# Kernel tuning notes

Measured on AMD Instinct MI355X. Metric: run time of the kernel, lower is better.

## Reference

```python
import jax, jax.numpy as jnp
import numpy as np

HALF_WIN = 6  # window_size // 2 on each side (window_size=13)


def setup_inputs() -> dict:
    key = jax.random.key(0)
    k1, k2, k3 = jax.random.split(key, 3)
    B, N, C = 2, 4096, 768
    x = jax.random.normal(k1, (B, N, C), dtype=jnp.float32)
    # torch Linear init ~ U(-1/sqrt(in), 1/sqrt(in)); stored here as [in, out]
    s = 1.0 / np.sqrt(C)
    w_qkv = jax.random.uniform(k2, (C, 3 * C), jnp.float32, -s, s)
    w_proj = jax.random.uniform(k3, (C, C), jnp.float32, -s, s)
    b_proj = jnp.zeros((C,), jnp.float32)
    return {"x": x, "w_qkv": w_qkv, "w_proj": w_proj, "b_proj": b_proj}


def _local_attn(x, w_qkv, w_proj, b_proj, num_heads=12):
    B, N, C = x.shape
    H = num_heads
    D = C // H
    W = 2 * HALF_WIN + 1  # 13

    qkv = (x @ w_qkv).reshape(B, N, 3, H, D)
    q, k, v = qkv[:, :, 0], qkv[:, :, 1], qkv[:, :, 2]  # each [B,N,H,D]

    # sliding-window gather: for each query i, keys at i-6..i+6
    offs = jnp.arange(-HALF_WIN, HALF_WIN + 1)            # [W]
    idx = jnp.arange(N)[:, None] + offs[None, :]          # [N,W]
    valid = (idx >= 0) & (idx < N)                        # [N,W]
    idxc = jnp.clip(idx, 0, N - 1)

    k_win = k[:, idxc]  # [B,N,W,H,D]
    v_win = v[:, idxc]  # [B,N,W,H,D]

    scale = D ** (-0.5)  # xformers default softmax scale
    scores = jnp.einsum('bnhd,bnwhd->bnhw', q, k_win) * scale  # [B,N,H,W]
    neg = jnp.asarray(jnp.finfo(scores.dtype).min, scores.dtype)
    scores = jnp.where(valid[None, :, None, :], scores, neg)
    p = jax.nn.softmax(scores, axis=-1)

    out = jnp.einsum('bnhw,bnwhd->bnhd', p, v_win)  # [B,N,H,D]
    out = out.reshape(B, N, C)
    return out @ w_proj + b_proj


def reference(x, w_qkv, w_proj, b_proj):
    return _local_attn(x, w_qkv, w_proj, b_proj)
```

## Files before the change

kernel.cpp:

```cpp
#include <hip/hip_runtime.h>

typedef unsigned short u16;
typedef unsigned int u32;
typedef __attribute__((ext_vector_type(8))) short short8;
typedef __attribute__((ext_vector_type(4))) float f32x4;

#define GLOBAL_AS(p) (const __attribute__((address_space(1))) void*)(p)
#define LDS_AS(p) (__attribute__((address_space(3))) void*)(p)

__device__ __forceinline__ u16 f2b(float f) {
  u32 u = __float_as_uint(f);
  u32 r = (u + 0x7fffu + ((u >> 16) & 1u)) >> 16;
  return (u16)r;
}
__device__ __forceinline__ float blo(u32 u) { return __uint_as_float(u << 16); }
__device__ __forceinline__ float bhi(u32 u) { return __uint_as_float(u & 0xffff0000u); }

__global__ void conv_bf16(const float* __restrict__ in, u16* __restrict__ out, int n4) {
  int i = blockIdx.x * blockDim.x + threadIdx.x;
  int stride = gridDim.x * blockDim.x;
  for (; i < n4; i += stride) {
    float4 f = ((const float4*)in)[i];
    ushort4 u;
    u.x = f2b(f.x); u.y = f2b(f.y); u.z = f2b(f.z); u.w = f2b(f.w);
    ((ushort4*)out)[i] = u;
  }
}

__global__ void transpose_conv2(const float* __restrict__ w_qkv, u16* __restrict__ wqT,
                                const float* __restrict__ w_proj, u16* __restrict__ wpT) {
  __shared__ float tile[32][33];
  const int z = blockIdx.z;
  if (z && blockIdx.x >= 24) return;
  const float* in = z ? w_proj : w_qkv;
  u16* out = z ? wpT : wqT;
  const int Cc = z ? 768 : 2304;
  int c0 = blockIdx.x * 32, r0 = blockIdx.y * 32;
  int tx = threadIdx.x, ty = threadIdx.y;
#pragma unroll
  for (int i = 0; i < 32; i += 8)
    tile[ty + i][tx] = in[(size_t)(r0 + ty + i) * Cc + c0 + tx];
  __syncthreads();
#pragma unroll
  for (int i = 0; i < 32; i += 8)
    out[(size_t)(c0 + ty + i) * 768 + r0 + tx] = f2b(tile[tx][ty + i]);
}


#define GLD(SRC, DST) __builtin_amdgcn_global_load_lds(GLOBAL_AS(SRC), LDS_AS(DST), 16, 0, 0)
#define WAITN(n) asm volatile("s_waitcnt vmcnt(" #n ")" ::: "memory")

#define WAITSEL                                                                          \
  do {                                                                                   \
    if (NBCH >= 1024) { if (wex) WAITN(7); else WAITN(6); }                              \
    else              { if (wex) WAITN(6); else WAITN(5); }                              \
  } while (0)

#define STAGEW(KT, SB)                                                                   \
  do {                                                                                   \
    const u16* a_ = gA0 + (KT) * 64;                                                     \
    GLD(a_,            lA + (SB) * 16384 + t * 8);                                       \
    GLD(a_ + 64 * kk,  lA + (SB) * 16384 + (t + 512) * 8);                               \
    GLD(a_ + 128 * kk, lA + (SB) * 16384 + (t + 1024) * 8);                              \
    GLD(a_ + 192 * kk, lA + (SB) * 16384 + (t + 1536) * 8);                              \
    const u16* b_ = gB0 + (KT) * 64;                                                     \
    GLD(b_, lB + (SB) * TBSZ + t * 8);                                                   \
    if (NBCH >= 1024) {                                                                  \
      GLD(b_ + 64 * kk, lB + (SB) * TBSZ + (t + 512) * 8);                               \
      if (t < NBCH - 1024) GLD(b_ + 128 * kk, lB + (SB) * TBSZ + (t + 1024) * 8);        \
    } else {                                                                             \
      if (t < NBCH - 512) GLD(b_ + 64 * kk, lB + (SB) * TBSZ + (t + 512) * 8);           \
    }                                                                                    \
  } while (0)

#define ITERW(KT, CB, SB, DOSTAGE, FINAL)                                                \
  do {                                                                                   \
    if (FINAL) WAITN(0); else WAITSEL;                                                   \
    __builtin_amdgcn_s_barrier();                                                        \
    asm volatile("" ::: "memory");                                                       \
    if (DOSTAGE) STAGEW((KT) + 2, SB);                                                   \
    const u16* pa_ = lA + (CB) * 16384;                                                  \
    const u16* pb_ = lB + (CB) * TBSZ;                                                   \
    {                                                                                    \
      short8 a0 = *(const short8*)(pa_ + arow0 + cs0);                                   \
      short8 a1 = *(const short8*)(pa_ + arow1 + cs0);                                   \
      short8 bf[NFRAG];                                                                  \
      _Pragma("unroll")                                                                  \
      for (int ni = 0; ni < NFRAG; ++ni)                                                 \
        bf[ni] = *(const short8*)(pb_ + ni * 1024 + browb + cs0);                        \
      __builtin_amdgcn_s_setprio(1);                                                     \
      _Pragma("unroll")                                                                  \
      for (int ni = 0; ni < NFRAG; ++ni) {                                               \
        acc[0][ni] = __builtin_amdgcn_mfma_f32_16x16x32_bf16(a0, bf[ni], acc[0][ni], 0, 0, 0); \
        acc[1][ni] = __builtin_amdgcn_mfma_f32_16x16x32_bf16(a1, bf[ni], acc[1][ni], 0, 0, 0); \
      }                                                                                  \
      __builtin_amdgcn_s_setprio(0);                                                     \
    }                                                                                    \
    {                                                                                    \
      short8 a0 = *(const short8*)(pa_ + arow0 + cs1);                                   \
      short8 a1 = *(const short8*)(pa_ + arow1 + cs1);                                   \
      short8 bf[NFRAG];                                                                  \
      _Pragma("unroll")                                                                  \
      for (int ni = 0; ni < NFRAG; ++ni)                                                 \
        bf[ni] = *(const short8*)(pb_ + ni * 1024 + browb + cs1);                        \
      __builtin_amdgcn_s_setprio(1);                                                     \
      _Pragma("unroll")                                                                  \
      for (int ni = 0; ni < NFRAG; ++ni) {                                               \
        acc[0][ni] = __builtin_amdgcn_mfma_f32_16x16x32_bf16(a0, bf[ni], acc[0][ni], 0, 0, 0); \
        acc[1][ni] = __builtin_amdgcn_mfma_f32_16x16x32_bf16(a1, bf[ni], acc[1][ni], 0, 0, 0); \
      }                                                                                  \
      __builtin_amdgcn_s_setprio(0);                                                     \
    }                                                                                    \
  } while (0)

template <int EPI, int NFRAG>
__global__ __launch_bounds__(512, 2) void gemmW(
    const u16* __restrict__ A, const u16* __restrict__ Bt, void* __restrict__ Cout,
    const float* __restrict__ bias, int M, int N, int K, int NXP) {
  constexpr int NBCH = NFRAG * 128;
  constexpr int TBSZ = NFRAG * 1024;
  constexpr int EXW = (NBCH >= 1024 ? NBCH - 1024 : NBCH - 512) / 64;
  extern __shared__ u16 sm[];
  u16* lA = sm;
  u16* lB = sm + 3 * 16384;
  const int t = threadIdx.x;
  const size_t kk = (size_t)K;
  const int nwg = gridDim.x;
  const int logical = (blockIdx.x & 7) * (nwg >> 3) + (blockIdx.x >> 3);
  const int m0 = (logical / NXP) * 256;
  const int n0 = (logical % NXP) * (NFRAG * 16);
  const int wv = t >> 6, l = t & 63;
  const int lr = l & 15, g = l >> 4;
  const bool wex = wv < EXW;

  const int ra = t >> 3;
  const int ca = (t & 7) ^ (ra & 7);
  const u16* gA0 = A + (size_t)(m0 + ra) * kk + ca * 8;
  const u16* gB0 = Bt + (size_t)(n0 + ra) * kk + ca * 8;

  const int cs0 = ((g + 0) ^ (lr & 7)) * 8;
  const int cs1 = ((g + 4) ^ (lr & 7)) * 8;
  const int arow0 = (wv * 32 + lr) * 64, arow1 = (wv * 32 + 16 + lr) * 64;
  const int browb = lr * 64;

  f32x4 acc[2][NFRAG] = {};

  STAGEW(0, 0);
  STAGEW(1, 1);
  for (int j = 0; j < 3; ++j) {
    const int kt = j * 3;
    ITERW(kt + 0, 0, 2, 1, 0);
    ITERW(kt + 1, 1, 0, 1, 0);
    ITERW(kt + 2, 2, 1, 1, 0);
  }
  ITERW(9, 0, 2, 1, 0);
  ITERW(10, 1, 2, 0, 0);
  ITERW(11, 2, 2, 0, 1);

#pragma unroll
  for (int mi = 0; mi < 2; ++mi) {
    int row = m0 + wv * 32 + mi * 16 + g * 4;
#pragma unroll
    for (int ni = 0; ni < NFRAG; ++ni) {
      int col = n0 + ni * 16 + lr;
#pragma unroll
      for (int r = 0; r < 4; ++r) {
        float v = acc[mi][ni][r];
        if (EPI == 0) {
          ((u16*)Cout)[(size_t)(row + r) * N + col] = f2b(v);
        } else {
          ((float*)Cout)[(size_t)(row + r) * N + col] = v + bias[col];
        }
      }
    }
  }
}

#define NTILE 128
#define ROWS 140
#define LPAD 66

__global__ __launch_bounds__(512, 6) void attn_kernel(const u16* __restrict__ qkv,
                                                      u16* __restrict__ attn) {
  const int nt = blockIdx.x, h = blockIdx.y, b = blockIdx.z;
  const int n0 = nt * NTILE;
  const int t = threadIdx.x;
  __shared__ u16 kl[ROWS * LPAD];
  __shared__ u16 vl[ROWS * LPAD];

  for (int i = t; i < 2 * ROWS * 8; i += 512) {
    int mat = i >= ROWS * 8;
    int j = mat ? i - ROWS * 8 : i;
    int r = j >> 3, c = j & 7;
    int grow = n0 - 6 + r;
    grow = grow < 0 ? 0 : (grow > 4095 ? 4095 : grow);
    const uint4 u =
        *(const uint4*)(qkv + (size_t)(b * 4096 + grow) * 2304 + (mat ? 1536 : 768) + h * 64 + c * 8);
    u16* dst = (mat ? vl : kl) + r * LPAD + c * 8;
    ((u32*)dst)[0] = u.x;
    ((u32*)dst)[1] = u.y;
    ((u32*)dst)[2] = u.z;
    ((u32*)dst)[3] = u.w;
  }
  __syncthreads();

  const int r = t >> 2;
  const int p = t & 3;
  const int n = n0 + r;
  const int dbase = p * 16;

  float qf[16];
  const u16* qp = qkv + (size_t)(b * 4096 + n) * 2304 + h * 64 + dbase;
#pragma unroll
  for (int c = 0; c < 2; ++c) {
    uint4 u = *(const uint4*)(qp + c * 8);
    qf[c * 8 + 0] = blo(u.x); qf[c * 8 + 1] = bhi(u.x);
    qf[c * 8 + 2] = blo(u.y); qf[c * 8 + 3] = bhi(u.y);
    qf[c * 8 + 4] = blo(u.z); qf[c * 8 + 5] = bhi(u.z);
    qf[c * 8 + 6] = blo(u.w); qf[c * 8 + 7] = bhi(u.w);
  }

  float s[13];
#pragma unroll
  for (int w = 0; w < 13; ++w) s[w] = 0.f;
#pragma unroll
  for (int d2 = 0; d2 < 8; ++d2) {
    float q0 = qf[2 * d2], q1 = qf[2 * d2 + 1];
#pragma unroll
    for (int w = 0; w < 13; ++w) {
      u32 u = *(const u32*)(kl + (r + w) * LPAD + dbase + 2 * d2);
      s[w] += q0 * blo(u) + q1 * bhi(u);
    }
  }
#pragma unroll
  for (int w = 0; w < 13; ++w) {
    s[w] += __shfl_xor(s[w], 1);
    s[w] += __shfl_xor(s[w], 2);
  }

#pragma unroll
  for (int w = 0; w < 13; ++w) {
    int nn = n - 6 + w;
    s[w] = (nn >= 0 && nn < 4096) ? s[w] * 0.125f : -1e30f;
  }
  float m = s[0];
#pragma unroll
  for (int w = 1; w < 13; ++w) m = fmaxf(m, s[w]);
  float sum = 0.f;
#pragma unroll
  for (int w = 0; w < 13; ++w) {
    float pr = __expf(s[w] - m);
    s[w] = pr;
    sum += pr;
  }
  float inv = 1.0f / sum;

  float o[16];
#pragma unroll
  for (int d = 0; d < 16; ++d) o[d] = 0.f;
#pragma unroll
  for (int w = 0; w < 13; ++w) {
    float pw = s[w] * inv;
#pragma unroll
    for (int d2 = 0; d2 < 8; ++d2) {
      u32 u = *(const u32*)(vl + (r + w) * LPAD + dbase + 2 * d2);
      o[2 * d2] += pw * blo(u);
      o[2 * d2 + 1] += pw * bhi(u);
    }
  }

  u16* op = attn + (size_t)(b * 4096 + n) * 768 + h * 64 + dbase;
#pragma unroll
  for (int c = 0; c < 2; ++c) {
    uint4 u;
    u.x = (u32)f2b(o[c * 8 + 0]) | ((u32)f2b(o[c * 8 + 1]) << 16);
    u.y = (u32)f2b(o[c * 8 + 2]) | ((u32)f2b(o[c * 8 + 3]) << 16);
    u.z = (u32)f2b(o[c * 8 + 4]) | ((u32)f2b(o[c * 8 + 5]) << 16);
    u.w = (u32)f2b(o[c * 8 + 6]) | ((u32)f2b(o[c * 8 + 7]) << 16);
    ((uint4*)op)[c] = u;
  }
}

extern "C" void kernel_launch(void* const* d_in, const int* in_sizes, int n_in,
                              void* d_out, int out_size, void* d_ws, size_t ws_size,
                              hipStream_t stream) {
  const float* x = (const float*)d_in[0];
  const float* w_qkv = (const float*)d_in[1];
  const float* w_proj = (const float*)d_in[2];
  const float* b_proj = (const float*)d_in[3];
  float* out = (float*)d_out;

  char* p = (char*)d_ws;
  u16* xb = (u16*)p;     p += (size_t)8192 * 768 * 2;
  u16* wqT = (u16*)p;    p += (size_t)2304 * 768 * 2;
  u16* wpT = (u16*)p;    p += (size_t)768 * 768 * 2;
  u16* qkvb = (u16*)p;   p += (size_t)8192 * 2304 * 2;
  u16* attnb = (u16*)p;  p += (size_t)8192 * 768 * 2;

  const int lds1 = 3 * (32768 + 18432);
  const int lds2 = 3 * (32768 + 12288);
  hipFuncSetAttribute((const void*)gemmW<0, 9>, hipFuncAttributeMaxDynamicSharedMemorySize, lds1);
  hipFuncSetAttribute((const void*)gemmW<1, 6>, hipFuncAttributeMaxDynamicSharedMemorySize, lds2);

  conv_bf16<<<dim3(2048), dim3(256), 0, stream>>>(x, xb, 8192 * 768 / 4);
  transpose_conv2<<<dim3(72, 24, 2), dim3(32, 8), 0, stream>>>(w_qkv, wqT, w_proj, wpT);

  gemmW<0, 9><<<dim3(512), dim3(512), lds1, stream>>>(
      xb, wqT, (void*)qkvb, nullptr, 8192, 2304, 768, 16);

  attn_kernel<<<dim3(4096 / NTILE, 12, 2), dim3(512), 0, stream>>>(qkvb, attnb);

  gemmW<1, 6><<<dim3(256), dim3(512), lds2, stream>>>(
      attnb, wpT, (void*)out, b_proj, 8192, 768, 768, 8);
}
```

Measured before the change: 151.2 us.

## Software-pipeline LDS fragment reads with MFMA via register double-buffering in GEMM

Restructures the GEMM main loop so LDS reads for the next half-tile go into a second register set while MFMAs run on the current one. The global-load wait and barrier move into the middle of each iteration, so the next buffer's first half is prefetched before the second-half MFMAs. This is meant to hide LDS read latency behind matrix-core work. It doubles the fragment registers held per thread, which at 512 threads with 2 blocks per CU could cause spills. The prologue and epilogue are hand-unrolled and must match the buffer rotation exactly.

New measurement: 158.5 us. 4.8% more time.

```diff
diff --git a/kernel.cpp b/kernel.cpp
--- a/kernel.cpp
+++ b/kernel.cpp
@@ -73,48 +73,44 @@
     }                                                                                    \
   } while (0)
 
-#define ITERW(KT, CB, SB, DOSTAGE, FINAL)                                                \
-  do {                                                                                   \
-    if (FINAL) WAITN(0); else WAITSEL;                                                   \
+#define READH(A0, A1, BARR, BUF, CS)                                                     \
+  do {                                                                                   \
+    const u16* pa_ = lA + (BUF) * 16384;                                                 \
+    const u16* pb_ = lB + (BUF) * TBSZ;                                                  \
+    A0 = *(const short8*)(pa_ + arow0 + (CS));                                           \
+    A1 = *(const short8*)(pa_ + arow1 + (CS));                                           \
+    _Pragma("unroll")                                                                    \
+    for (int ni = 0; ni < NFRAG; ++ni)                                                   \
+      BARR[ni] = *(const short8*)(pb_ + ni * 1024 + browb + (CS));                       \
+  } while (0)
+
+#define MFMA2N(A0, A1, BARR)                                                             \
+  do {                                                                                   \
+    __builtin_amdgcn_s_setprio(1);                                                       \
+    _Pragma("unroll")                                                                    \
+    for (int ni = 0; ni < NFRAG; ++ni) {                                                 \
+      acc[0][ni] = __builtin_amdgcn_mfma_f32_16x16x32_bf16(A0, BARR[ni], acc[0][ni], 0, 0, 0); \
+      acc[1][ni] = __builtin_amdgcn_mfma_f32_16x16x32_bf16(A1, BARR[ni], acc[1][ni], 0, 0, 0); \
+    }                                                                                    \
+    __builtin_amdgcn_s_setprio(0);                                                       \
+  } while (0)
+
+#define ITERP(KT, CB, NB, SB)                                                            \
+  do {                                                                                   \
     __builtin_amdgcn_s_barrier();                                                        \
     asm volatile("" ::: "memory");                                                       \
-    if (DOSTAGE) STAGEW((KT) + 2, SB);                                                   \
-    const u16* pa_ = lA + (CB) * 16384;                                                  \
-    const u16* pb_ = lB + (CB) * TBSZ;                                                   \
-    {                                                                                    \
-      short8 a0 = *(const short8*)(pa_ + arow0 + cs0);                                   \
-      short8 a1 = *(const short8*)(pa_ + arow1 + cs0);                                   \
-      short8 bf[NFRAG];                                                                  \
-      _Pragma("unroll")                                                                  \
-      for (int ni = 0; ni < NFRAG; ++ni)                                                 \
-        bf[ni] = *(const short8*)(pb_ + ni * 1024 + browb + cs0);                        \
-      __builtin_amdgcn_s_setprio(1);                                                     \
-      _Pragma("unroll")                                                                  \
-      for (int ni = 0; ni < NFRAG; ++ni) {                                               \
-        acc[0][ni] = __builtin_amdgcn_mfma_f32_16x16x32_bf16(a0, bf[ni], acc[0][ni], 0, 0, 0); \
-        acc[1][ni] = __builtin_amdgcn_mfma_f32_16x16x32_bf16(a1, bf[ni], acc[1][ni], 0, 0, 0); \
-      }                                                                                  \
-      __builtin_amdgcn_s_setprio(0);                                                     \
-    }                                                                                    \
-    {                                                                                    \
-      short8 a0 = *(const short8*)(pa_ + arow0 + cs1);                                   \
-      short8 a1 = *(const short8*)(pa_ + arow1 + cs1);                                   \
-      short8 bf[NFRAG];                                                                  \
-      _Pragma("unroll")                                                                  \
-      for (int ni = 0; ni < NFRAG; ++ni)                                                 \
-        bf[ni] = *(const short8*)(pb_ + ni * 1024 + browb + cs1);                        \
-      __builtin_amdgcn_s_setprio(1);                                                     \
-      _Pragma("unroll")                                                                  \
-      for (int ni = 0; ni < NFRAG; ++ni) {                                               \
-        acc[0][ni] = __builtin_amdgcn_mfma_f32_16x16x32_bf16(a0, bf[ni], acc[0][ni], 0, 0, 0); \
-        acc[1][ni] = __builtin_amdgcn_mfma_f32_16x16x32_bf16(a1, bf[ni], acc[1][ni], 0, 0, 0); \
-      }                                                                                  \
-      __builtin_amdgcn_s_setprio(0);                                                     \
-    }                                                                                    \
+    STAGEW((KT) + 2, SB);                                                                \
+    READH(xA0, xA1, xB, CB, cs1);                                     \
+    MFMA2N(cA0, cA1, cB);                                             \
+    WAITSEL;                                          \
+    __builtin_amdgcn_s_barrier();                           \
+    asm volatile("" ::: "memory");                                                       \
+    READH(cA0, cA1, cB, NB, cs0);                      \
+    MFMA2N(xA0, xA1, xB);                                             \
   } while (0)
 
 template <int EPI, int NFRAG>
-__global__ __launch_bounds__(512, 2) void gemmW(
+__global__ __launch_bounds__(512, 2) void gemmP(
     const u16* __restrict__ A, const u16* __restrict__ Bt, void* __restrict__ Cout,
     const float* __restrict__ bias, int M, int N, int K, int NXP) {
   constexpr int NBCH = NFRAG * 128;
@@ -144,18 +140,33 @@
   const int browb = lr * 64;
 
   f32x4 acc[2][NFRAG] = {};
+  short8 cA0, cA1, cB[NFRAG], xA0, xA1, xB[NFRAG];
 
   STAGEW(0, 0);
   STAGEW(1, 1);
+  WAITSEL;
+  __builtin_amdgcn_s_barrier();
+  asm volatile("" ::: "memory");
+  READH(cA0, cA1, cB, 0, cs0);
+
+  int kt = 0;
   for (int j = 0; j < 3; ++j) {
-    const int kt = j * 3;
-    ITERW(kt + 0, 0, 2, 1, 0);
-    ITERW(kt + 1, 1, 0, 1, 0);
-    ITERW(kt + 2, 2, 1, 1, 0);
-  }
-  ITERW(9, 0, 2, 1, 0);
-  ITERW(10, 1, 2, 0, 0);
-  ITERW(11, 2, 2, 0, 1);
+    ITERP(kt, 0, 1, 2); ++kt;
+    ITERP(kt, 1, 2, 0); ++kt;
+    ITERP(kt, 2, 0, 1); ++kt;
+  }
+  ITERP(9, 0, 1, 2);
+
+  READH(xA0, xA1, xB, 1, cs1);
+  MFMA2N(cA0, cA1, cB);
+  WAITN(0);
+  __builtin_amdgcn_s_barrier();
+  asm volatile("" ::: "memory");
+  READH(cA0, cA1, cB, 2, cs0);
+  MFMA2N(xA0, xA1, xB);
+  READH(xA0, xA1, xB, 2, cs1);
+  MFMA2N(cA0, cA1, cB);
+  MFMA2N(xA0, xA1, xB);
 
 #pragma unroll
   for (int mi = 0; mi < 2; ++mi) {
@@ -299,17 +310,17 @@
 
   const int lds1 = 3 * (32768 + 18432);
   const int lds2 = 3 * (32768 + 12288);
-  hipFuncSetAttribute((const void*)gemmW<0, 9>, hipFuncAttributeMaxDynamicSharedMemorySize, lds1);
-  hipFuncSetAttribute((const void*)gemmW<1, 6>, hipFuncAttributeMaxDynamicSharedMemorySize, lds2);
+  hipFuncSetAttribute((const void*)gemmP<0, 9>, hipFuncAttributeMaxDynamicSharedMemorySize, lds1);
+  hipFuncSetAttribute((const void*)gemmP<1, 6>, hipFuncAttributeMaxDynamicSharedMemorySize, lds2);
 
   conv_bf16<<<dim3(2048), dim3(256), 0, stream>>>(x, xb, 8192 * 768 / 4);
   transpose_conv2<<<dim3(72, 24, 2), dim3(32, 8), 0, stream>>>(w_qkv, wqT, w_proj, wpT);
 
-  gemmW<0, 9><<<dim3(512), dim3(512), lds1, stream>>>(
+  gemmP<0, 9><<<dim3(512), dim3(512), lds1, stream>>>(
       xb, wqT, (void*)qkvb, nullptr, 8192, 2304, 768, 16);
 
   attn_kernel<<<dim3(4096 / NTILE, 12, 2), dim3(512), 0, stream>>>(qkvb, attnb);
 
-  gemmW<1, 6><<<dim3(256), dim3(512), lds2, stream>>>(
+  gemmP<1, 6><<<dim3(256), dim3(512), lds2, stream>>>(
       attnb, wpT, (void*)out, b_proj, 8192, 768, 768, 8);
 }
```
